# Kernel tuning notes

Hardware: AMD Instinct MI355X
Metric: run time of the kernel (lower is better)

## Reference

```python
import jax, jax.numpy as jnp
import numpy as np

K = 5  # kNN neighbors (includes self, as in PyG knn(x, x, k))


def _lin_bn(x, W, b, s, h):
    # Linear -> ReLU -> BatchNorm (inference, folded to scale s / shift h)
    return jax.nn.relu(x @ W + b) * s + h


def _knn_idx(x, k):
    # x: [B, N, F] -> idx: [B, N, k] indices of k nearest points (incl. self)
    x2 = jnp.sum(x * x, axis=-1)  # [B, N]
    d = x2[:, :, None] + x2[:, None, :] - 2.0 * jnp.einsum('bnf,bmf->bnm', x, x)
    return jax.lax.top_k(-d, k)[1]


def _edge_conv(x, k, edge_mlp):
    # DynamicEdgeConv: knn graph, message mlp([x_i, x_j - x_i]), max-aggregate
    idx = _knn_idx(x, k)                                   # [B, N, k]
    xj = jax.vmap(lambda xb, ib: xb[ib])(x, idx)           # [B, N, k, F]
    xi = jnp.broadcast_to(x[:, :, None, :], xj.shape)
    e = jnp.concatenate([xi, xj - xi], axis=-1)            # [B, N, k, 2F]
    return jnp.max(edge_mlp(e), axis=2)                    # [B, N, F_out]


def _forward(pos, w1a, b1a, s1a, h1a, w1b, b1b, s1b, h1b, w1c, b1c, s1c, h1c,
             w2, b2, s2, h2, wl, bl, sl, hl,
             wm1, bm1, sm1, hm1, wm2, bm2, sm2, hm2, wout, bout):
    mlp1 = lambda e: _lin_bn(_lin_bn(_lin_bn(e, w1a, b1a, s1a, h1a),
                                     w1b, b1b, s1b, h1b), w1c, b1c, s1c, h1c)
    mlp2 = lambda e: _lin_bn(e, w2, b2, s2, h2)
    x1 = _edge_conv(pos, K, mlp1)                          # [B, N, 64]
    x2 = _edge_conv(x1, K, mlp2)                           # [B, N, 128]
    out = _lin_bn(jnp.concatenate([x1, x2], axis=-1), wl, bl, sl, hl)  # [B,N,1024]
    out = jnp.max(out, axis=1)                             # global max pool -> [B,1024]
    out = _lin_bn(out, wm1, bm1, sm1, hm1)                 # Dropout = identity (eval)
    out = _lin_bn(out, wm2, bm2, sm2, hm2)
    return out @ wout + bout                               # [B, n_classes]


def setup_inputs() -> dict:
    key = jax.random.key(0)
    ks = jax.random.split(key, 32)
    B, N = 32, 2048
    rn = lambda k, sh: jax.random.normal(k, sh, dtype=jnp.float32)
    ru = lambda k, sh: jax.random.uniform(k, sh, dtype=jnp.float32)
    d = {'pos': rn(ks[0], (B, N, 3))}
    i = 1
    for nm, cin, cout in [('1a', 6, 64), ('1b', 64, 64), ('1c', 64, 64),
                          ('2', 128, 128), ('l', 192, 1024),
                          ('m1', 1024, 512), ('m2', 512, 256)]:
        d['w' + nm] = rn(ks[i], (cin, cout)) / np.sqrt(cin); i += 1
        d['b' + nm] = rn(ks[i], (cout,)) * 0.1; i += 1
        d['s' + nm] = ru(ks[i], (cout,)) + 0.5; i += 1
        d['h' + nm] = rn(ks[i], (cout,)) * 0.1; i += 1
    d['wout'] = rn(ks[i], (256, 2)) / np.sqrt(256.0); i += 1
    d['bout'] = rn(ks[i], (2,)) * 0.1
    return d


def reference(pos, w1a, b1a, s1a, h1a, w1b, b1b, s1b, h1b, w1c, b1c, s1c, h1c,
              w2, b2, s2, h2, wl, bl, sl, hl,
              wm1, bm1, sm1, hm1, wm2, bm2, sm2, hm2, wout, bout):
    return _forward(pos, w1a, b1a, s1a, h1a, w1b, b1b, s1b, h1b, w1c, b1c, s1c, h1c,
                    w2, b2, s2, h2, wl, bl, sl, hl,
                    wm1, bm1, sm1, hm1, wm2, bm2, sm2, hm2, wout, bout)
```

## Files before the change

### kernel.cpp

```cpp
#include <hip/hip_runtime.h>

#define DEV __device__ __forceinline__
DEV float relu_(float x) { return fmaxf(x, 0.0f); }

typedef __attribute__((ext_vector_type(4))) float f32x4;
typedef __attribute__((ext_vector_type(8))) __bf16 bf16x8;

DEV unsigned short bfbits(__bf16 b) { union { unsigned short s; __bf16 b; } x; x.b = b; return x.s; }
DEV __bf16 bffrom(unsigned short s) { union { unsigned short s; __bf16 b; } x; x.s = s; return x.b; }

DEV void knn_insert(float (&bd)[5], int (&bi)[5], float d, int j) {
  if (d >= bd[4]) return;
  bd[4] = d; bi[4] = j;
#pragma unroll
  for (int p = 4; p > 0; --p) {
    if (bd[p] < bd[p - 1]) {
      float td = bd[p]; bd[p] = bd[p - 1]; bd[p - 1] = td;
      int ti = bi[p]; bi[p] = bi[p - 1]; bi[p - 1] = ti;
    }
  }
}

DEV void knn_insert_bl(float (&bd)[5], int (&bi)[5], float d, int j) {
#pragma unroll
  for (int p = 0; p < 5; ++p) {
    bool lt = d < bd[p];
    float nd = lt ? d : bd[p];
    float cd = lt ? bd[p] : d;
    int ni = lt ? j : bi[p];
    int ci = lt ? bi[p] : j;
    bd[p] = nd; d = cd;
    bi[p] = ni; j = ci;
  }
}

DEV void ins5(float (&b)[5], float x) {
  b[4] = __builtin_amdgcn_fmed3f(b[3], b[4], x);
  b[3] = __builtin_amdgcn_fmed3f(b[2], b[3], x);
  b[2] = __builtin_amdgcn_fmed3f(b[1], b[2], x);
  b[1] = __builtin_amdgcn_fmed3f(b[0], b[1], x);
  b[0] = fminf(b[0], x);
}

__global__ __launch_bounds__(256) void k_front(
    const float* __restrict__ pos, const float* __restrict__ w1a,
    const float* __restrict__ b1a, const float* __restrict__ w1b,
    const float* __restrict__ w1c, const float* __restrict__ w2,
    const float* __restrict__ wl,
    int* __restrict__ idx1, float* __restrict__ uR, float* __restrict__ vR,
    __bf16* __restrict__ wfh, __bf16* __restrict__ wfl,
    __bf16* __restrict__ wph, __bf16* __restrict__ wpl,
    __bf16* __restrict__ wlb) {
  __shared__ __align__(16) float smem[9472];
  int tid = threadIdx.x;
  int blk = blockIdx.x;
  if (blk < 2048) {
    float* ps = smem;
    float* sqs = smem + 6144;
    float* md = smem + 8192;
    int* mi = (int*)(smem + 8832);
    int b = blk >> 6, qc = blk & 63;
    const float* src = pos + b * 6144;
    for (int u = tid; u < 6144; u += 256) ps[u] = src[u];
    __syncthreads();
    for (int u = tid; u < 2048; u += 256) {
      float x = ps[u * 3], y = ps[u * 3 + 1], z = ps[u * 3 + 2];
      sqs[u] = fmaf(z, z, fmaf(y, y, x * x));
    }
    __syncthreads();
    int q = tid & 31, sub = tid >> 5;
    int qi = qc * 32 + q;
    float qx = ps[qi * 3], qy = ps[qi * 3 + 1], qz = ps[qi * 3 + 2];
    float qsq = sqs[qi];
    float bp[5] = {1e30f, 1e30f, 1e30f, 1e30f, 1e30f};
    int j0 = sub * 256;
    for (int j = j0; j < j0 + 256; ++j) {
      float px = ps[j * 3], py = ps[j * 3 + 1], pz = ps[j * 3 + 2];
      float dot = fmaf(qz, pz, fmaf(qy, py, qx * px));
      float d = fmaxf((qsq + sqs[j]) - 2.0f * dot, 0.0f);
      unsigned u = (__float_as_uint(d) & 0xFFFFFF00u) | (unsigned)(j & 255);
      ins5(bp, __uint_as_float(u));
    }
    float bd[5]; int bi[5];
#pragma unroll
    for (int k = 0; k < 5; ++k) {
      unsigned u = __float_as_uint(bp[k]);
      bd[k] = __uint_as_float(u & 0xFFFFFF00u);
      bi[k] = j0 + (int)(u & 255u);
    }
    for (int half = 4; half >= 1; half >>= 1) {
      __syncthreads();
      if (sub >= half && sub < 2 * half) {
        int slot = (q * 4 + (sub - half)) * 5;
#pragma unroll
        for (int k = 0; k < 5; ++k) { md[slot + k] = bd[k]; mi[slot + k] = bi[k]; }
      }
      __syncthreads();
      if (sub < half) {
        int slot = (q * 4 + sub) * 5;
#pragma unroll
        for (int k = 0; k < 5; ++k) knn_insert_bl(bd, bi, md[slot + k], mi[slot + k]);
      }
    }
    if (sub == 0) {
      int* op = idx1 + (b * 2048 + qi) * 5;
#pragma unroll
      for (int k = 0; k < 5; ++k) op[k] = bi[k];
    }
  } else if (blk < 3072) {
    float* wAs = smem;
    float* bs = smem + 384;
    float* uS = smem + 448;
    float* vS = smem + 4800;
    for (int u = tid; u < 384; u += 256) wAs[u] = w1a[u];
    if (tid < 64) bs[tid] = b1a[tid];
    __syncthreads();
    int lane = tid & 63, fq = tid >> 6;
    int p0 = (blk - 2048) * 64;
    int p = p0 + lane;
    float x0 = pos[p * 3], x1 = pos[p * 3 + 1], x2 = pos[p * 3 + 2];
#pragma unroll
    for (int m = 0; m < 16; ++m) {
      int f = fq * 16 + m;
      float wt0 = wAs[f], wt1 = wAs[64 + f], wt2 = wAs[128 + f];
      float wb0 = wAs[192 + f], wb1 = wAs[256 + f], wb2 = wAs[320 + f];
      float uval = bs[f];
      uval = fmaf(x0, wt0 - wb0, uval);
      uval = fmaf(x1, wt1 - wb1, uval);
      uval = fmaf(x2, wt2 - wb2, uval);
      uS[lane * 68 + f] = uval;
      vS[lane * 68 + f] = fmaf(x2, wb2, fmaf(x1, wb1, x0 * wb0));
    }
    __syncthreads();
#pragma unroll
    for (int it = 0; it < 4; ++it) {
      int g = it * 1024 + tid * 4;
      int pl = g >> 6, f = g & 63;
      float4 uu = *(const float4*)(uS + pl * 68 + f);
      float4 vv = *(const float4*)(vS + pl * 68 + f);
      *(float4*)(uR + (size_t)p0 * 64 + g) = uu;
      *(float4*)(vR + (size_t)p0 * 64 + g) = vv;
    }
  } else {
    int pblk = blk - 3072;
    if (pblk < 4) {
      int t = pblk * 256 + tid;
      int m = t >> 9;
      int rem = t & 511;
      int nb = rem >> 7;
      int rem2 = rem & 127;
      int s = rem2 >> 6, lane = rem2 & 63;
      int k0 = s * 32 + (lane >> 4) * 8;
      int c = nb * 16 + (lane & 15);
      const float* W = m ? w1c : w1b;
      __bf16 oh[8], ol[8];
#pragma unroll
      for (int j = 0; j < 8; ++j) {
        float val = W[(k0 + j) * 64 + c];
        __bf16 h = (__bf16)val;
        oh[j] = h;
        ol[j] = (__bf16)(val - (float)h);
      }
      size_t off = (size_t)m * 4096 + ((size_t)((nb * 2 + s) * 64 + lane)) * 8;
      *(uint4*)(wfh + off) = *(const uint4*)oh;
      *(uint4*)(wfl + off) = *(const uint4*)ol;
    } else if (pblk < 12) {
      int t = (pblk - 4) * 256 + tid;
      int nb = t >> 7;
      int rem = t & 127;
      int ks = rem >> 6, lane = rem & 63;
      int k0 = ks * 32 + (lane >> 4) * 8;
      int col16 = lane & 15;
      __bf16 oh[8], ol[8];
#pragma unroll
      for (int j = 0; j < 8; ++j) {
        int k = k0 + j;
        float val;
        if (nb < 8) {
          int c = nb * 16 + col16;
          val = w2[k * 128 + c] - w2[(64 + k) * 128 + c];
        } else {
          int c = (nb - 8) * 16 + col16;
          val = w2[(64 + k) * 128 + c];
        }
        __bf16 h = (__bf16)val;
        oh[j] = h;
        ol[j] = (__bf16)(val - (float)h);
      }
      *(uint4*)(wph + (size_t)t * 8) = *(const uint4*)oh;
      *(uint4*)(wpl + (size_t)t * 8) = *(const uint4*)ol;
    } else {
      int t = (pblk - 12) * 256 + tid;
      int nt = t / 3072;
      int rem = t - nt * 3072;
      int ks = rem / 512;
      int rem2 = rem - ks * 512;
      int nb = rem2 >> 6, lane = rem2 & 63;
      int k0 = ks * 32 + (lane >> 4) * 8;
      int n = nt * 128 + nb * 16 + (lane & 15);
      __bf16 o[8];
#pragma unroll
      for (int j = 0; j < 8; ++j) o[j] = (__bf16)wl[(k0 + j) * 1024 + n];
      *(uint4*)(wlb + (size_t)t * 8) = *(const uint4*)o;
    }
  }
}

__global__ __launch_bounds__(256) void k_edge1(
    const int* __restrict__ idx1, const float* __restrict__ uR,
    const float* __restrict__ vR,
    const float* __restrict__ s1a, const float* __restrict__ h1a,
    const float* __restrict__ b1b, const float* __restrict__ s1b,
    const float* __restrict__ h1b,
    const float* __restrict__ b1c, const float* __restrict__ s1c,
    const float* __restrict__ h1c,
    const __bf16* __restrict__ wfh, const __bf16* __restrict__ wfl,
    __bf16* __restrict__ xh, __bf16* __restrict__ xl,
    float* __restrict__ sqo, __bf16* __restrict__ xb) {
  __shared__ __align__(16) __bf16 Wh[8192], Wl[8192];
  __shared__ __align__(16) unsigned h2b[4 * 1088];
  int tid = threadIdx.x;
  int w = tid >> 6, lane = tid & 63;
  int quad = lane >> 4, lm = lane & 15;
#pragma unroll
  for (int it = 0; it < 4; ++it) {
    int u4 = it * 256 + tid;
    *(uint4*)(Wh + (size_t)u4 * 8) = *(const uint4*)(wfh + (size_t)u4 * 8);
    *(uint4*)(Wl + (size_t)u4 * 8) = *(const uint4*)(wfl + (size_t)u4 * 8);
  }
  int p0 = blockIdx.x * 64;
  int b = p0 >> 11;
  size_t bb = (size_t)b * 2048;
  int edge = p0 + w * 16 + lm;
  float sA[2][8], hA[2][8];
#pragma unroll
  for (int s = 0; s < 2; ++s)
#pragma unroll
    for (int j = 0; j < 8; ++j) {
      int k = s * 32 + quad * 8 + j;
      sA[s][j] = s1a[k]; hA[s][j] = h1a[k];
    }
  float bB[4], sB[4], hB[4], bC[4], sC[4], hC[4];
#pragma unroll
  for (int nb = 0; nb < 4; ++nb) {
    int c = nb * 16 + lm;
    bB[nb] = b1b[c]; sB[nb] = s1b[c]; hB[nb] = h1b[c];
    bC[nb] = b1c[c]; sC[nb] = s1c[c]; hC[nb] = h1c[c];
  }
  unsigned* h2w = h2b + w * 1088;
  f32x4 mmax[4];
#pragma unroll
  for (int nb = 0; nb < 4; ++nb)
    mmax[nb] = (f32x4){-3.4e38f, -3.4e38f, -3.4e38f, -3.4e38f};
  __syncthreads();
  const float* urow = uR + (size_t)edge * 64;
  for (int kk = 0; kk < 5; ++kk) {
    int jn = idx1[edge * 5 + kk];
    const float* vrow = vR + (bb + jn) * 64;
    bf16x8 Ah[2], Al[2];
#pragma unroll
    for (int s = 0; s < 2; ++s) {
      int off = s * 32 + quad * 8;
      float4 u0 = *(const float4*)(urow + off);
      float4 u1 = *(const float4*)(urow + off + 4);
      float4 v0 = *(const float4*)(vrow + off);
      float4 v1 = *(const float4*)(vrow + off + 4);
      float uv[8] = {u0.x + v0.x, u0.y + v0.y, u0.z + v0.z, u0.w + v0.w,
                     u1.x + v1.x, u1.y + v1.y, u1.z + v1.z, u1.w + v1.w};
      __bf16 th[8], tl[8];
#pragma unroll
      for (int j = 0; j < 8; ++j) {
        float val = relu_(uv[j]) * sA[s][j] + hA[s][j];
        __bf16 hb = (__bf16)val;
        th[j] = hb;
        tl[j] = (__bf16)(val - (float)hb);
      }
      Ah[s] = *(const bf16x8*)th;
      Al[s] = *(const bf16x8*)tl;
    }
#pragma unroll
    for (int nb = 0; nb < 4; ++nb) {
      bf16x8 Bh0 = *(const bf16x8*)(Wh + ((size_t)((nb * 2 + 0) * 64 + lane)) * 8);
      bf16x8 Bh1 = *(const bf16x8*)(Wh + ((size_t)((nb * 2 + 1) * 64 + lane)) * 8);
      bf16x8 Bl0 = *(const bf16x8*)(Wl + ((size_t)((nb * 2 + 0) * 64 + lane)) * 8);
      bf16x8 Bl1 = *(const bf16x8*)(Wl + ((size_t)((nb * 2 + 1) * 64 + lane)) * 8);
      f32x4 a2 = {0.f, 0.f, 0.f, 0.f};
      a2 = __builtin_amdgcn_mfma_f32_16x16x32_bf16(Ah[0], Bh0, a2, 0, 0, 0);
      a2 = __builtin_amdgcn_mfma_f32_16x16x32_bf16(Ah[1], Bh1, a2, 0, 0, 0);
      a2 = __builtin_amdgcn_mfma_f32_16x16x32_bf16(Ah[0], Bl0, a2, 0, 0, 0);
      a2 = __builtin_amdgcn_mfma_f32_16x16x32_bf16(Ah[1], Bl1, a2, 0, 0, 0);
      a2 = __builtin_amdgcn_mfma_f32_16x16x32_bf16(Al[0], Bh0, a2, 0, 0, 0);
      a2 = __builtin_amdgcn_mfma_f32_16x16x32_bf16(Al[1], Bh1, a2, 0, 0, 0);
#pragma unroll
      for (int r = 0; r < 4; ++r) {
        float vv2 = relu_(a2[r] + bB[nb]) * sB[nb] + hB[nb];
        __bf16 hb = (__bf16)vv2;
        __bf16 lb = (__bf16)(vv2 - (float)hb);
        h2w[(quad * 4 + r) * 68 + nb * 16 + lm] =
            (unsigned)bfbits(hb) | ((unsigned)bfbits(lb) << 16);
      }
    }
    bf16x8 A3h[2], A3l[2];
#pragma unroll
    for (int s = 0; s < 2; ++s) {
      const unsigned* rp = h2w + lm * 68 + s * 32 + quad * 8;
      uint4 da = *(const uint4*)rp;
      uint4 db = *(const uint4*)(rp + 4);
      unsigned dw[8] = {da.x, da.y, da.z, da.w, db.x, db.y, db.z, db.w};
      __bf16 th[8], tl[8];
#pragma unroll
      for (int j = 0; j < 8; ++j) {
        th[j] = bffrom((unsigned short)(dw[j] & 0xFFFFu));
        tl[j] = bffrom((unsigned short)(dw[j] >> 16));
      }
      A3h[s] = *(const bf16x8*)th;
      A3l[s] = *(const bf16x8*)tl;
    }
#pragma unroll
    for (int nb = 0; nb < 4; ++nb) {
      bf16x8 Bh0 = *(const bf16x8*)(Wh + 4096 + ((size_t)((nb * 2 + 0) * 64 + lane)) * 8);
      bf16x8 Bh1 = *(const bf16x8*)(Wh + 4096 + ((size_t)((nb * 2 + 1) * 64 + lane)) * 8);
      bf16x8 Bl0 = *(const bf16x8*)(Wl + 4096 + ((size_t)((nb * 2 + 0) * 64 + lane)) * 8);
      bf16x8 Bl1 = *(const bf16x8*)(Wl + 4096 + ((size_t)((nb * 2 + 1) * 64 + lane)) * 8);
      f32x4 a3 = {0.f, 0.f, 0.f, 0.f};
      a3 = __builtin_amdgcn_mfma_f32_16x16x32_bf16(A3h[0], Bh0, a3, 0, 0, 0);
      a3 = __builtin_amdgcn_mfma_f32_16x16x32_bf16(A3h[1], Bh1, a3, 0, 0, 0);
      a3 = __builtin_amdgcn_mfma_f32_16x16x32_bf16(A3h[0], Bl0, a3, 0, 0, 0);
      a3 = __builtin_amdgcn_mfma_f32_16x16x32_bf16(A3h[1], Bl1, a3, 0, 0, 0);
      a3 = __builtin_amdgcn_mfma_f32_16x16x32_bf16(A3l[0], Bh0, a3, 0, 0, 0);
      a3 = __builtin_amdgcn_mfma_f32_16x16x32_bf16(A3l[1], Bh1, a3, 0, 0, 0);
#pragma unroll
      for (int r = 0; r < 4; ++r) mmax[nb][r] = fmaxf(mmax[nb][r], a3[r]);
    }
  }
  float sqp[4] = {0.f, 0.f, 0.f, 0.f};
#pragma unroll
  for (int nb = 0; nb < 4; ++nb) {
    int c = nb * 16 + lm;
#pragma unroll
    for (int r = 0; r < 4; ++r) {
      float vv3 = relu_(mmax[nb][r] + bC[nb]) * sC[nb] + hC[nb];
      sqp[r] = fmaf(vv3, vv3, sqp[r]);
      __bf16 hb = (__bf16)vv3;
      __bf16 lb = (__bf16)(vv3 - (float)hb);
      int n = p0 + w * 16 + quad * 4 + r;
      xh[(size_t)n * 64 + c] = hb;
      xl[(size_t)n * 64 + c] = lb;
      xb[(size_t)n * 192 + c] = hb;
    }
  }
#pragma unroll
  for (int r = 0; r < 4; ++r) {
    float s = sqp[r];
    s += __shfl_xor(s, 1);
    s += __shfl_xor(s, 2);
    s += __shfl_xor(s, 4);
    s += __shfl_xor(s, 8);
    if (lm == 0) sqo[p0 + w * 16 + quad * 4 + r] = s;
  }
}

__global__ __launch_bounds__(256) void k_mid(const __bf16* __restrict__ xh,
                                             const __bf16* __restrict__ xl,
                                             const float* __restrict__ sq,
                                             int* __restrict__ idx2,
                                             const __bf16* __restrict__ wph,
                                             const __bf16* __restrict__ wpl,
                                             __bf16* __restrict__ Pb,
                                             __bf16* __restrict__ Qb) {
  __shared__ __align__(16) float smem[6656];
  int tid = threadIdx.x;
  int w = tid >> 6, lane = tid & 63;
  int quad = lane >> 4, lm = lane & 15;
  if (blockIdx.x < 1024) {
    __bf16* Bh = (__bf16*)smem;
    __bf16* Bl = (__bf16*)(smem + 2304);
    float* sqs = smem + 4608;
    int b = blockIdx.x >> 5, qc = blockIdx.x & 31;
    int q0 = qc * 64;
    size_t bb = (size_t)b * 2048;
    for (int u = tid; u < 512; u += 256)
      *(float4*)(sqs + u * 4) = *(const float4*)(sq + bb + u * 4);
    const __bf16* qh = xh + (bb + q0 + w * 16 + lm) * 64 + quad * 8;
    const __bf16* ql = xl + (bb + q0 + w * 16 + lm) * 64 + quad * 8;
    bf16x8 Ah0 = *(const bf16x8*)(qh);
    bf16x8 Ah1 = *(const bf16x8*)(qh + 32);
    bf16x8 Al0 = *(const bf16x8*)(ql);
    bf16x8 Al1 = *(const bf16x8*)(ql + 32);
    __syncthreads();
    float qsq[4];
#pragma unroll
    for (int r = 0; r < 4; ++r) qsq[r] = sqs[q0 + w * 16 + quad * 4 + r];
    float bp[4][5];
#pragma unroll
    for (int r = 0; r < 4; ++r)
#pragma unroll
      for (int k = 0; k < 5; ++k) bp[r][k] = 1e30f;
    for (int ct = 0; ct < 32; ++ct) {
#pragma unroll
      for (int pass = 0; pass < 2; ++pass) {
        int unit = pass * 256 + tid;
        int n = unit >> 3, cc = unit & 7;
        const __bf16* gsrc = xh + (bb + ct * 64 + n) * 64 + cc * 8;
        const __bf16* gsrl = xl + (bb + ct * 64 + n) * 64 + cc * 8;
        *(uint4*)(Bh + n * 72 + cc * 8) = *(const uint4*)gsrc;
        *(uint4*)(Bl + n * 72 + cc * 8) = *(const uint4*)gsrl;
      }
      __syncthreads();
#pragma unroll
      for (int nt = 0; nt < 4; ++nt) {
        const __bf16* bph = Bh + (nt * 16 + lm) * 72 + quad * 8;
        const __bf16* bpl = Bl + (nt * 16 + lm) * 72 + quad * 8;
        bf16x8 Bh0 = *(const bf16x8*)(bph);
        bf16x8 Bh1 = *(const bf16x8*)(bph + 32);
        bf16x8 Bl0 = *(const bf16x8*)(bpl);
        bf16x8 Bl1 = *(const bf16x8*)(bpl + 32);
        f32x4 acc = {0.f, 0.f, 0.f, 0.f};
        acc = __builtin_amdgcn_mfma_f32_16x16x32_bf16(Ah0, Bh0, acc, 0, 0, 0);
        acc = __builtin_amdgcn_mfma_f32_16x16x32_bf16(Ah1, Bh1, acc, 0, 0, 0);
        acc = __builtin_amdgcn_mfma_f32_16x16x32_bf16(Ah0, Bl0, acc, 0, 0, 0);
        acc = __builtin_amdgcn_mfma_f32_16x16x32_bf16(Ah1, Bl1, acc, 0, 0, 0);
        acc = __builtin_amdgcn_mfma_f32_16x16x32_bf16(Al0, Bh0, acc, 0, 0, 0);
        acc = __builtin_amdgcn_mfma_f32_16x16x32_bf16(Al1, Bh1, acc, 0, 0, 0);
        int cid = ct * 64 + nt * 16 + lm;
        float csq = sqs[cid];
        unsigned key = (unsigned)(ct * 4 + nt);
#pragma unroll
        for (int r = 0; r < 4; ++r) {
          float d = fmaxf((qsq[r] + csq) - 2.0f * acc[r], 0.0f);
          unsigned u = (__float_as_uint(d) & 0xFFFFFF80u) | key;
          ins5(bp[r], __uint_as_float(u));
        }
      }
      __syncthreads();
    }
    float bd[4][5];
    int bi[4][5];
#pragma unroll
    for (int r = 0; r < 4; ++r)
#pragma unroll
      for (int k = 0; k < 5; ++k) {
        unsigned u = __float_as_uint(bp[r][k]);
        bd[r][k] = __uint_as_float(u & 0xFFFFFF80u);
        bi[r][k] = (int)((u & 0x7Fu) << 4) | lm;
      }
    for (int m = 1; m <= 8; m <<= 1) {
#pragma unroll
      for (int r = 0; r < 4; ++r) {
        float od[5]; int oi[5];
#pragma unroll
        for (int k = 0; k < 5; ++k) {
          od[k] = __shfl_xor(bd[r][k], m);
          oi[k] = __shfl_xor(bi[r][k], m);
        }
#pragma unroll
        for (int k = 0; k < 5; ++k) knn_insert(bd[r], bi[r], od[k], oi[k]);
      }
    }
    if (lm == 0) {
#pragma unroll
      for (int r = 0; r < 4; ++r) {
        int qi = q0 + w * 16 + quad * 4 + r;
        int* op = idx2 + (bb + qi) * 5;
#pragma unroll
        for (int k = 0; k < 5; ++k) op[k] = bi[r][k];
      }
    }
  } else {
    __bf16* Wh = (__bf16*)smem;
    __bf16* Wl = (__bf16*)(smem + 2048);
    int n0 = (blockIdx.x - 1024) * 64;
    const __bf16* ah = xh + (size_t)(n0 + w * 16 + lm) * 64 + quad * 8;
    const __bf16* al = xl + (size_t)(n0 + w * 16 + lm) * 64 + quad * 8;
    bf16x8 Ah0 = *(const bf16x8*)(ah);
    bf16x8 Ah1 = *(const bf16x8*)(ah + 32);
    bf16x8 Al0 = *(const bf16x8*)(al);
    bf16x8 Al1 = *(const bf16x8*)(al + 32);
    for (int chunk = 0; chunk < 4; ++chunk) {
      __syncthreads();
#pragma unroll
      for (int it = 0; it < 2; ++it) {
        int unit = it * 256 + tid;
        *(uint4*)(Wh + (size_t)unit * 8) =
            *(const uint4*)(wph + (size_t)chunk * 4096 + (size_t)unit * 8);
        *(uint4*)(Wl + (size_t)unit * 8) =
            *(const uint4*)(wpl + (size_t)chunk * 4096 + (size_t)unit * 8);
      }
      __syncthreads();
#pragma unroll
      for (int nb4 = 0; nb4 < 4; ++nb4) {
        int nb = chunk * 4 + nb4;
        bf16x8 Bh0 = *(const bf16x8*)(Wh + ((size_t)(nb4 * 2 + 0) * 64 + lane) * 8);
        bf16x8 Bh1 = *(const bf16x8*)(Wh + ((size_t)(nb4 * 2 + 1) * 64 + lane) * 8);
        bf16x8 Bl0 = *(const bf16x8*)(Wl + ((size_t)(nb4 * 2 + 0) * 64 + lane) * 8);
        bf16x8 Bl1 = *(const bf16x8*)(Wl + ((size_t)(nb4 * 2 + 1) * 64 + lane) * 8);
        f32x4 acc = {0.f, 0.f, 0.f, 0.f};
        acc = __builtin_amdgcn_mfma_f32_16x16x32_bf16(Ah0, Bh0, acc, 0, 0, 0);
        acc = __builtin_amdgcn_mfma_f32_16x16x32_bf16(Ah1, Bh1, acc, 0, 0, 0);
        acc = __builtin_amdgcn_mfma_f32_16x16x32_bf16(Ah0, Bl0, acc, 0, 0, 0);
        acc = __builtin_amdgcn_mfma_f32_16x16x32_bf16(Ah1, Bl1, acc, 0, 0, 0);
        acc = __builtin_amdgcn_mfma_f32_16x16x32_bf16(Al0, Bh0, acc, 0, 0, 0);
        acc = __builtin_amdgcn_mfma_f32_16x16x32_bf16(Al1, Bh1, acc, 0, 0, 0);
        bool isP = (nb < 8);
        __bf16* base = isP ? Pb : Qb;
        int col = (isP ? nb : nb - 8) * 16 + lm;
#pragma unroll
        for (int r = 0; r < 4; ++r) {
          int n = n0 + w * 16 + quad * 4 + r;
          base[(size_t)n * 128 + col] = (__bf16)acc[r];
        }
      }
    }
  }
}

__global__ __launch_bounds__(256) void k_gmax(const __bf16* __restrict__ Pb,
                                              const __bf16* __restrict__ Qb,
                                              const int* __restrict__ idx2,
                                              const float* __restrict__ b2,
                                              const float* __restrict__ s2,
                                              const float* __restrict__ h2v,
                                              __bf16* __restrict__ xb) {
  int tid = threadIdx.x;
  int c4 = tid & 31, p = tid >> 5;
  int n = blockIdx.x * 8 + p;
  int b = n >> 11;
  const int* ip = idx2 + n * 5;
  int c0 = c4 * 4;
  float m[4] = {-3.4e38f, -3.4e38f, -3.4e38f, -3.4e38f};
#pragma unroll
  for (int k = 0; k < 5; ++k) {
    int j = ip[k];
    uint2 q = *(const uint2*)(Qb + ((size_t)(b * 2048 + j)) * 128 + c0);
    m[0] = fmaxf(m[0], (float)bffrom((unsigned short)(q.x & 0xFFFFu)));
    m[1] = fmaxf(m[1], (float)bffrom((unsigned short)(q.x >> 16)));
    m[2] = fmaxf(m[2], (float)bffrom((unsigned short)(q.y & 0xFFFFu)));
    m[3] = fmaxf(m[3], (float)bffrom((unsigned short)(q.y >> 16)));
  }
  uint2 pv = *(const uint2*)(Pb + (size_t)n * 128 + c0);
  float pvf[4] = {(float)bffrom((unsigned short)(pv.x & 0xFFFFu)),
                  (float)bffrom((unsigned short)(pv.x >> 16)),
                  (float)bffrom((unsigned short)(pv.y & 0xFFFFu)),
                  (float)bffrom((unsigned short)(pv.y >> 16))};
  __bf16 o[4];
#pragma unroll
  for (int i = 0; i < 4; ++i) {
    float v = pvf[i] + m[i] + b2[c0 + i];
    o[i] = (__bf16)(relu_(v) * s2[c0 + i] + h2v[c0 + i]);
  }
  uint2 ov;
  ov.x = (unsigned)bfbits(o[0]) | ((unsigned)bfbits(o[1]) << 16);
  ov.y = (unsigned)bfbits(o[2]) | ((unsigned)bfbits(o[3]) << 16);
  *(uint2*)(xb + (size_t)n * 192 + 64 + c0) = ov;
}

__global__ __launch_bounds__(256) void k_linl_mfma(const __bf16* __restrict__ xb,
                                                   const __bf16* __restrict__ wlb,
                                                   float* __restrict__ pool_part) {
  __shared__ __align__(16) __bf16 Aall[12288];
  __shared__ __align__(16) __bf16 Bl[8192];
  int tid = threadIdx.x;
  int w = tid >> 6, lane = tid & 63;
  int mg = blockIdx.x;
  int n0 = mg << 6;
  int quad = lane >> 4, lm = lane & 15;
#pragma unroll
  for (int it = 0; it < 6; ++it) {
    int unit = it * 256 + tid;
    int mb = unit / 384;
    int rem = unit - mb * 384;
    int ks = rem >> 6, ln = rem & 63;
    int lmm = ln & 15, qd = ln >> 4;
    const uint4* ga = (const uint4*)(xb + (size_t)(n0 + mb * 16 + lmm) * 192 + ks * 32 + qd * 8);
    *(uint4*)(Aall + ((size_t)(mb * 6 + ks) * 64 + ln) * 8) = *ga;
  }
  for (int ng = 0; ng < 4; ++ng) {
    f32x4 acc[4][4];
#pragma unroll
    for (int i = 0; i < 4; ++i)
#pragma unroll
      for (int j = 0; j < 4; ++j) acc[i][j] = (f32x4){0.f, 0.f, 0.f, 0.f};
    for (int ks = 0; ks < 6; ++ks) {
      __syncthreads();
#pragma unroll
      for (int nt2 = 0; nt2 < 2; ++nt2) {
#pragma unroll
        for (int u = 0; u < 2; ++u) {
          int unit = u * 256 + tid;
          const uint4* gb = (const uint4*)(wlb + ((size_t)((ng * 2 + nt2) * 6 + ks)) * 4096 + (size_t)unit * 8);
          *(uint4*)(Bl + (size_t)nt2 * 4096 + (size_t)unit * 8) = *gb;
        }
      }
      __syncthreads();
      bf16x8 af[4], bfr[4];
#pragma unroll
      for (int i = 0; i < 4; ++i)
        af[i] = *(const bf16x8*)(Aall + ((size_t)(i * 6 + ks) * 64 + lane) * 8);
      int nt2 = w >> 1, nbb = (w & 1) * 4;
#pragma unroll
      for (int j = 0; j < 4; ++j)
        bfr[j] = *(const bf16x8*)(Bl + (size_t)nt2 * 4096 + ((size_t)((nbb + j) * 64 + lane)) * 8);
#pragma unroll
      for (int i = 0; i < 4; ++i)
#pragma unroll
        for (int j = 0; j < 4; ++j)
          acc[i][j] = __builtin_amdgcn_mfma_f32_16x16x32_bf16(af[i], bfr[j], acc[i][j], 0, 0, 0);
    }
#pragma unroll
    for (int j = 0; j < 4; ++j) {
      float m = -3.4e38f;
#pragma unroll
      for (int i = 0; i < 4; ++i)
#pragma unroll
        for (int r = 0; r < 4; ++r) m = fmaxf(m, acc[i][j][r]);
      m = fmaxf(m, __shfl_xor(m, 16));
      m = fmaxf(m, __shfl_xor(m, 32));
      if (quad == 0) {
        int ch = ng * 256 + (w >> 1) * 128 + (w & 1) * 64 + j * 16 + lm;
        pool_part[(size_t)mg * 1024 + ch] = m;
      }
    }
  }
}

__global__ __launch_bounds__(256) void k_pool(const float* __restrict__ pool_part,
                                              const float* __restrict__ bl,
                                              const float* __restrict__ sl,
                                              const float* __restrict__ hl,
                                              float* __restrict__ p,
                                              float* __restrict__ out) {
  int b = blockIdx.x >> 2, cb = blockIdx.x & 3;
  int c = cb * 256 + threadIdx.x;
  const float* src = pool_part + (size_t)(b * 32) * 1024 + c;
  float m0 = -3.4e38f, m1 = -3.4e38f, m2 = -3.4e38f, m3 = -3.4e38f;
#pragma unroll
  for (int t = 0; t < 32; t += 4) {
    m0 = fmaxf(m0, src[(size_t)t * 1024]);
    m1 = fmaxf(m1, src[(size_t)(t + 1) * 1024]);
    m2 = fmaxf(m2, src[(size_t)(t + 2) * 1024]);
    m3 = fmaxf(m3, src[(size_t)(t + 3) * 1024]);
  }
  float m = fmaxf(fmaxf(m0, m1), fmaxf(m2, m3));
  p[b * 1024 + c] = relu_(m + bl[c]) * sl[c] + hl[c];
  if (blockIdx.x == 0 && threadIdx.x < 64) out[threadIdx.x] = 0.0f;
}

__global__ __launch_bounds__(256) void k_m1(const float* __restrict__ p,
                                            const float* __restrict__ wm1,
                                            const float* __restrict__ bm1,
                                            const float* __restrict__ sm1,
                                            const float* __restrict__ hm1,
                                            float* __restrict__ h1) {
  __shared__ float p_s[1024];
  __shared__ float red[4][64];
  int b = blockIdx.x >> 3, cb = blockIdx.x & 7;
  int tid = threadIdx.x;
  for (int u = tid; u < 1024; u += 256) p_s[u] = p[b * 1024 + u];
  __syncthreads();
  int c64 = tid & 63, q = tid >> 6;
  int C = cb * 64 + c64;
  int f0 = q * 256;
  const float* W = wm1 + (size_t)f0 * 512 + C;
  float a[8] = {0.f, 0.f, 0.f, 0.f, 0.f, 0.f, 0.f, 0.f};
  for (int f = 0; f < 256; f += 8) {
#pragma unroll
    for (int u = 0; u < 8; ++u)
      a[u] = fmaf(p_s[f0 + f + u], W[(size_t)(f + u) * 512], a[u]);
  }
  red[q][c64] = ((a[0] + a[1]) + (a[2] + a[3])) + ((a[4] + a[5]) + (a[6] + a[7]));
  __syncthreads();
  if (tid < 64) {
    float t = (red[0][tid] + red[1][tid]) + (red[2][tid] + red[3][tid]);
    int C2 = cb * 64 + tid;
    h1[b * 512 + C2] = relu_(t + bm1[C2]) * sm1[C2] + hm1[C2];
  }
}

__global__ __launch_bounds__(256) void k_m2o(const float* __restrict__ h1,
                                             const float* __restrict__ wm2,
                                             const float* __restrict__ bm2,
                                             const float* __restrict__ sm2,
                                             const float* __restrict__ hm2,
                                             const float* __restrict__ wout,
                                             const float* __restrict__ bout,
                                             float* __restrict__ out) {
  __shared__ float h1_s[512];
  __shared__ float red[4][64];
  int b = blockIdx.x >> 2, cb = blockIdx.x & 3;
  int tid = threadIdx.x;
  for (int u = tid; u < 512; u += 256) h1_s[u] = h1[b * 512 + u];
  __syncthreads();
  int c64 = tid & 63, q = tid >> 6;
  int C = cb * 64 + c64;
  int f0 = q * 128;
  const float* W = wm2 + (size_t)f0 * 256 + C;
  float a[4] = {0.f, 0.f, 0.f, 0.f};
  for (int f = 0; f < 128; f += 4) {
#pragma unroll
    for (int u = 0; u < 4; ++u)
      a[u] = fmaf(h1_s[f0 + f + u], W[(size_t)(f + u) * 256], a[u]);
  }
  red[q][c64] = (a[0] + a[1]) + (a[2] + a[3]);
  __syncthreads();
  if (tid < 64) {
    float t = (red[0][tid] + red[1][tid]) + (red[2][tid] + red[3][tid]);
    int C2 = cb * 64 + tid;
    float h2v = relu_(t + bm2[C2]) * sm2[C2] + hm2[C2];
    float2 wv = *(const float2*)(wout + C2 * 2);
    float v0 = h2v * wv.x, v1 = h2v * wv.y;
#pragma unroll
    for (int m = 1; m < 64; m <<= 1) {
      v0 += __shfl_xor(v0, m);
      v1 += __shfl_xor(v1, m);
    }
    if (tid == 0) {
      if (cb == 0) { v0 += bout[0]; v1 += bout[1]; }
      atomicAdd(&out[b * 2], v0);
      atomicAdd(&out[b * 2 + 1], v1);
    }
  }
}

extern "C" void kernel_launch(void* const* d_in, const int* in_sizes, int n_in,
                              void* d_out, int out_size, void* d_ws, size_t ws_size,
                              hipStream_t stream) {
  const float* pos = (const float*)d_in[0];
  const float* w1a = (const float*)d_in[1];
  const float* b1a = (const float*)d_in[2];
  const float* s1a = (const float*)d_in[3];
  const float* h1a = (const float*)d_in[4];
  const float* w1b = (const float*)d_in[5];
  const float* b1b = (const float*)d_in[6];
  const float* s1b = (const float*)d_in[7];
  const float* h1b = (const float*)d_in[8];
  const float* w1c = (const float*)d_in[9];
  const float* b1c = (const float*)d_in[10];
  const float* s1c = (const float*)d_in[11];
  const float* h1c = (const float*)d_in[12];
  const float* w2 = (const float*)d_in[13];
  const float* b2 = (const float*)d_in[14];
  const float* s2 = (const float*)d_in[15];
  const float* h2 = (const float*)d_in[16];
  const float* wl = (const float*)d_in[17];
  const float* bl = (const float*)d_in[18];
  const float* sl = (const float*)d_in[19];
  const float* hl = (const float*)d_in[20];
  const float* wm1 = (const float*)d_in[21];
  const float* bm1 = (const float*)d_in[22];
  const float* sm1 = (const float*)d_in[23];
  const float* hm1 = (const float*)d_in[24];
  const float* wm2 = (const float*)d_in[25];
  const float* bm2 = (const float*)d_in[26];
  const float* sm2 = (const float*)d_in[27];
  const float* hm2 = (const float*)d_in[28];
  const float* wout = (const float*)d_in[29];
  const float* bout = (const float*)d_in[30];
  float* out = (float*)d_out;

  float* base = (float*)d_ws;
  __bf16* xh = (__bf16*)base;
  __bf16* xl = (__bf16*)(base + 2097152);
  float* PbF = base + 4194304;
  float* QbF = PbF + 4194304;
  float* xbF = QbF + 4194304;
  int* idx = (int*)(xbF + 6291456);
  float* sq = (float*)(idx + 327680);
  __bf16* wph = (__bf16*)(sq + 65536);
  __bf16* wpl = (__bf16*)(sq + 65536 + 8192);
  __bf16* wfh = (__bf16*)(sq + 65536 + 16384);
  __bf16* wfl = (__bf16*)(sq + 65536 + 20480);
  __bf16* wlb = (__bf16*)(sq + 65536 + 24576);
  __bf16* Pb = (__bf16*)PbF;
  __bf16* Qb = (__bf16*)QbF;
  __bf16* xb = (__bf16*)xbF;
  float* uR = PbF;
  float* vR = QbF;
  float* pool_part = base + 131072;
  float* p_pool = base + 1179648;
  float* h1g = base + 1212416;

  k_front<<<3180, 256, 0, stream>>>(pos, w1a, b1a, w1b, w1c, w2, wl, idx, uR, vR,
                                    wfh, wfl, wph, wpl, wlb);
  k_edge1<<<1024, 256, 0, stream>>>(idx, uR, vR, s1a, h1a, b1b, s1b, h1b, b1c,
                                    s1c, h1c, wfh, wfl, xh, xl, sq, xb);
  k_mid<<<2048, 256, 0, stream>>>(xh, xl, sq, idx, wph, wpl, Pb, Qb);
  k_gmax<<<8192, 256, 0, stream>>>(Pb, Qb, idx, b2, s2, h2, xb);
  k_linl_mfma<<<1024, 256, 0, stream>>>(xb, wlb, pool_part);
  k_pool<<<128, 256, 0, stream>>>(pool_part, bl, sl, hl, p_pool, out);
  k_m1<<<256, 256, 0, stream>>>(p_pool, wm1, bm1, sm1, hm1, h1g);
  k_m2o<<<128, 256, 0, stream>>>(h1g, wm2, bm2, sm2, hm2, wout, bout, out);
}
```

Measured before the change: 358.8 us.

## Split k_mid candidate scan across two thread groups with shared-memory top-k merge

k_mid now launches 512 threads per block. Two 256-thread groups each scan half of the candidate tiles (or half of the weight chunks in the projection branch) using their own shared-memory buffers. In the kNN branch, group 1 writes its per-row top-5 into shared memory and group 0 merges it before writing indices. This doubles per-block parallelism to shorten the serial candidate loop. In exchange it shrinks the key field in the packed distance to 6 bits, costs an extra merge and barrier, and raises shared-memory and register pressure per block.

```diff
diff --git a/kernel.cpp b/kernel.cpp
--- a/kernel.cpp
+++ b/kernel.cpp
@@ -360,7 +360,7 @@
   }
 }
 
-__global__ __launch_bounds__(256) void k_mid(const __bf16* __restrict__ xh,
+__global__ __launch_bounds__(512) void k_mid(const __bf16* __restrict__ xh,
                                              const __bf16* __restrict__ xl,
                                              const float* __restrict__ sq,
                                              int* __restrict__ idx2,
@@ -368,21 +368,23 @@
                                              const __bf16* __restrict__ wpl,
                                              __bf16* __restrict__ Pb,
                                              __bf16* __restrict__ Qb) {
-  __shared__ __align__(16) float smem[6656];
+  __shared__ __align__(16) float smem[11264];
   int tid = threadIdx.x;
-  int w = tid >> 6, lane = tid & 63;
+  int g = tid >> 8;
+  int t = tid & 255;
+  int ww = t >> 6;
+  int lane = tid & 63;
   int quad = lane >> 4, lm = lane & 15;
   if (blockIdx.x < 1024) {
-    __bf16* Bh = (__bf16*)smem;
-    __bf16* Bl = (__bf16*)(smem + 2304);
-    float* sqs = smem + 4608;
+    __bf16* Bh = (__bf16*)(smem + g * 4608);
+    __bf16* Bl = (__bf16*)(smem + g * 4608 + 2304);
+    float* sqs = smem + 9216;
     int b = blockIdx.x >> 5, qc = blockIdx.x & 31;
     int q0 = qc * 64;
     size_t bb = (size_t)b * 2048;
-    for (int u = tid; u < 512; u += 256)
-      *(float4*)(sqs + u * 4) = *(const float4*)(sq + bb + u * 4);
-    const __bf16* qh = xh + (bb + q0 + w * 16 + lm) * 64 + quad * 8;
-    const __bf16* ql = xl + (bb + q0 + w * 16 + lm) * 64 + quad * 8;
+    *(float4*)(sqs + tid * 4) = *(const float4*)(sq + bb + tid * 4);
+    const __bf16* qh = xh + (bb + q0 + ww * 16 + lm) * 64 + quad * 8;
+    const __bf16* ql = xl + (bb + q0 + ww * 16 + lm) * 64 + quad * 8;
     bf16x8 Ah0 = *(const bf16x8*)(qh);
     bf16x8 Ah1 = *(const bf16x8*)(qh + 32);
     bf16x8 Al0 = *(const bf16x8*)(ql);
@@ -390,16 +392,17 @@
     __syncthreads();
     float qsq[4];
 #pragma unroll
-    for (int r = 0; r < 4; ++r) qsq[r] = sqs[q0 + w * 16 + quad * 4 + r];
+    for (int r = 0; r < 4; ++r) qsq[r] = sqs[q0 + ww * 16 + quad * 4 + r];
     float bp[4][5];
 #pragma unroll
     for (int r = 0; r < 4; ++r)
 #pragma unroll
       for (int k = 0; k < 5; ++k) bp[r][k] = 1e30f;
-    for (int ct = 0; ct < 32; ++ct) {
+    for (int it = 0; it < 16; ++it) {
+      int ct = g * 16 + it;
 #pragma unroll
       for (int pass = 0; pass < 2; ++pass) {
-        int unit = pass * 256 + tid;
+        int unit = pass * 256 + t;
         int n = unit >> 3, cc = unit & 7;
         const __bf16* gsrc = xh + (bb + ct * 64 + n) * 64 + cc * 8;
         const __bf16* gsrl = xl + (bb + ct * 64 + n) * 64 + cc * 8;
@@ -422,13 +425,12 @@
         acc = __builtin_amdgcn_mfma_f32_16x16x32_bf16(Ah1, Bl1, acc, 0, 0, 0);
         acc = __builtin_amdgcn_mfma_f32_16x16x32_bf16(Al0, Bh0, acc, 0, 0, 0);
         acc = __builtin_amdgcn_mfma_f32_16x16x32_bf16(Al1, Bh1, acc, 0, 0, 0);
-        int cid = ct * 64 + nt * 16 + lm;
-        float csq = sqs[cid];
-        unsigned key = (unsigned)(ct * 4 + nt);
+        float csq = sqs[ct * 64 + nt * 16 + lm];
+        unsigned key = (unsigned)(it * 4 + nt);
 #pragma unroll
         for (int r = 0; r < 4; ++r) {
           float d = fmaxf((qsq[r] + csq) - 2.0f * acc[r], 0.0f);
-          unsigned u = (__float_as_uint(d) & 0xFFFFFF80u) | key;
+          unsigned u = (__float_as_uint(d) & 0xFFFFFFC0u) | key;
           ins5(bp[r], __uint_as_float(u));
         }
       }
@@ -441,8 +443,8 @@
 #pragma unroll
       for (int k = 0; k < 5; ++k) {
         unsigned u = __float_as_uint(bp[r][k]);
-        bd[r][k] = __uint_as_float(u & 0xFFFFFF80u);
-        bi[r][k] = (int)((u & 0x7Fu) << 4) | lm;
+        bd[r][k] = __uint_as_float(u & 0xFFFFFFC0u);
+        bi[r][k] = (((int)(u & 63u)) << 4) + lm + (g << 10);
       }
     for (int m = 1; m <= 8; m <<= 1) {
 #pragma unroll
@@ -457,30 +459,50 @@
         for (int k = 0; k < 5; ++k) knn_insert(bd[r], bi[r], od[k], oi[k]);
       }
     }
-    if (lm == 0) {
+    float* md = smem;
+    int* mi = (int*)(smem + 320);
+    if (g == 1 && lm == 0) {
 #pragma unroll
       for (int r = 0; r < 4; ++r) {
-        int qi = q0 + w * 16 + quad * 4 + r;
-        int* op = idx2 + (bb + qi) * 5;
-#pragma unroll
-        for (int k = 0; k < 5; ++k) op[k] = bi[r][k];
+        int row = ww * 16 + quad * 4 + r;
+#pragma unroll
+        for (int k = 0; k < 5; ++k) { md[row * 5 + k] = bd[r][k]; mi[row * 5 + k] = bi[r][k]; }
+      }
+    }
+    __syncthreads();
+    if (g == 0) {
+#pragma unroll
+      for (int r = 0; r < 4; ++r) {
+        int row = ww * 16 + quad * 4 + r;
+#pragma unroll
+        for (int k = 0; k < 5; ++k) knn_insert(bd[r], bi[r], md[row * 5 + k], mi[row * 5 + k]);
+      }
+      if (lm == 0) {
+#pragma unroll
+        for (int r = 0; r < 4; ++r) {
+          int qi = q0 + ww * 16 + quad * 4 + r;
+          int* op = idx2 + (bb + qi) * 5;
+#pragma unroll
+          for (int k = 0; k < 5; ++k) op[k] = bi[r][k];
+        }
       }
     }
   } else {
-    __bf16* Wh = (__bf16*)smem;
-    __bf16* Wl = (__bf16*)(smem + 2048);
+    __bf16* Wh = (__bf16*)(smem + g * 4096);
+    __bf16* Wl = (__bf16*)(smem + g * 4096 + 2048);
     int n0 = (blockIdx.x - 1024) * 64;
-    const __bf16* ah = xh + (size_t)(n0 + w * 16 + lm) * 64 + quad * 8;
-    const __bf16* al = xl + (size_t)(n0 + w * 16 + lm) * 64 + quad * 8;
+    const __bf16* ah = xh + (size_t)(n0 + ww * 16 + lm) * 64 + quad * 8;
+    const __bf16* al = xl + (size_t)(n0 + ww * 16 + lm) * 64 + quad * 8;
     bf16x8 Ah0 = *(const bf16x8*)(ah);
     bf16x8 Ah1 = *(const bf16x8*)(ah + 32);
     bf16x8 Al0 = *(const bf16x8*)(al);
     bf16x8 Al1 = *(const bf16x8*)(al + 32);
-    for (int chunk = 0; chunk < 4; ++chunk) {
+    for (int c2 = 0; c2 < 2; ++c2) {
+      int chunk = g * 2 + c2;
       __syncthreads();
 #pragma unroll
       for (int it = 0; it < 2; ++it) {
-        int unit = it * 256 + tid;
+        int unit = it * 256 + t;
         *(uint4*)(Wh + (size_t)unit * 8) =
             *(const uint4*)(wph + (size_t)chunk * 4096 + (size_t)unit * 8);
         *(uint4*)(Wl + (size_t)unit * 8) =
@@ -506,7 +528,7 @@
         int col = (isP ? nb : nb - 8) * 16 + lm;
 #pragma unroll
         for (int r = 0; r < 4; ++r) {
-          int n = n0 + w * 16 + quad * 4 + r;
+          int n = n0 + ww * 16 + quad * 4 + r;
           base[(size_t)n * 128 + col] = (__bf16)acc[r];
         }
       }
@@ -783,7 +805,7 @@
                                     wfh, wfl, wph, wpl, wlb);
   k_edge1<<<1024, 256, 0, stream>>>(idx, uR, vR, s1a, h1a, b1b, s1b, h1b, b1c,
                                     s1c, h1c, wfh, wfl, xh, xl, sq, xb);
-  k_mid<<<2048, 256, 0, stream>>>(xh, xl, sq, idx, wph, wpl, Pb, Qb);
+  k_mid<<<2048, 512, 0, stream>>>(xh, xl, sq, idx, wph, wpl, Pb, Qb);
   k_gmax<<<8192, 256, 0, stream>>>(Pb, Qb, idx, b2, s2, h2, xb);
   k_linl_mfma<<<1024, 256, 0, stream>>>(xb, wlb, pool_part);
   k_pool<<<128, 256, 0, stream>>>(pool_part, bl, sl, hl, p_pool, out);
```

Measured after the change: 375.0 us. 1.04x slower.

## Split second kNN candidate range across two blocks and merge partial top-5

Applied to the files above, without the earlier changes.

The second-layer kNN search now divides each query tile's 2048 candidates into two halves handled by separate blocks, which doubles the kNN grid from 1024 to 2048 blocks. Each block writes its partial top-5 distances and indices into an unused region of the xb buffer, and a new small kernel merges the two lists into the final indices. The aim is more parallelism and shorter per-block serial loops for better GPU occupancy. The cost is an extra kernel launch, scratch traffic, and one fewer key bit in the packed distance (mask 0xFFFFFFC0), which slightly coarsens distance precision.

```diff
diff --git a/kernel.cpp b/kernel.cpp
--- a/kernel.cpp
+++ b/kernel.cpp
@@ -363,7 +363,7 @@
 __global__ __launch_bounds__(256) void k_mid(const __bf16* __restrict__ xh,
                                              const __bf16* __restrict__ xl,
                                              const float* __restrict__ sq,
-                                             int* __restrict__ idx2,
+                                             __bf16* __restrict__ scratch,
                                              const __bf16* __restrict__ wph,
                                              const __bf16* __restrict__ wpl,
                                              __bf16* __restrict__ Pb,
@@ -372,11 +372,14 @@
   int tid = threadIdx.x;
   int w = tid >> 6, lane = tid & 63;
   int quad = lane >> 4, lm = lane & 15;
-  if (blockIdx.x < 1024) {
+  if (blockIdx.x < 2048) {
     __bf16* Bh = (__bf16*)smem;
     __bf16* Bl = (__bf16*)(smem + 2304);
     float* sqs = smem + 4608;
-    int b = blockIdx.x >> 5, qc = blockIdx.x & 31;
+    int blk = blockIdx.x;
+    int b = blk >> 6;
+    int w6 = blk & 63;
+    int qc = w6 >> 1, g = w6 & 1;
     int q0 = qc * 64;
     size_t bb = (size_t)b * 2048;
     for (int u = tid; u < 512; u += 256)
@@ -396,7 +399,8 @@
     for (int r = 0; r < 4; ++r)
 #pragma unroll
       for (int k = 0; k < 5; ++k) bp[r][k] = 1e30f;
-    for (int ct = 0; ct < 32; ++ct) {
+    for (int it = 0; it < 16; ++it) {
+      int ct = g * 16 + it;
 #pragma unroll
       for (int pass = 0; pass < 2; ++pass) {
         int unit = pass * 256 + tid;
@@ -422,13 +426,12 @@
         acc = __builtin_amdgcn_mfma_f32_16x16x32_bf16(Ah1, Bl1, acc, 0, 0, 0);
         acc = __builtin_amdgcn_mfma_f32_16x16x32_bf16(Al0, Bh0, acc, 0, 0, 0);
         acc = __builtin_amdgcn_mfma_f32_16x16x32_bf16(Al1, Bh1, acc, 0, 0, 0);
-        int cid = ct * 64 + nt * 16 + lm;
-        float csq = sqs[cid];
-        unsigned key = (unsigned)(ct * 4 + nt);
+        float csq = sqs[ct * 64 + nt * 16 + lm];
+        unsigned key = (unsigned)(it * 4 + nt);
 #pragma unroll
         for (int r = 0; r < 4; ++r) {
           float d = fmaxf((qsq[r] + csq) - 2.0f * acc[r], 0.0f);
-          unsigned u = (__float_as_uint(d) & 0xFFFFFF80u) | key;
+          unsigned u = (__float_as_uint(d) & 0xFFFFFFC0u) | key;
           ins5(bp[r], __uint_as_float(u));
         }
       }
@@ -441,8 +444,8 @@
 #pragma unroll
       for (int k = 0; k < 5; ++k) {
         unsigned u = __float_as_uint(bp[r][k]);
-        bd[r][k] = __uint_as_float(u & 0xFFFFFF80u);
-        bi[r][k] = (int)((u & 0x7Fu) << 4) | lm;
+        bd[r][k] = __uint_as_float(u & 0xFFFFFFC0u);
+        bi[r][k] = (g << 10) + (((int)(u & 63u)) << 4) + lm;
       }
     for (int m = 1; m <= 8; m <<= 1) {
 #pragma unroll
@@ -461,15 +464,20 @@
 #pragma unroll
       for (int r = 0; r < 4; ++r) {
         int qi = q0 + w * 16 + quad * 4 + r;
-        int* op = idx2 + (bb + qi) * 5;
-#pragma unroll
-        for (int k = 0; k < 5; ++k) op[k] = bi[r][k];
+        uint2* sp = (uint2*)((char*)scratch + (size_t)(bb + qi) * 384 + 128 + g * 40);
+#pragma unroll
+        for (int k = 0; k < 5; ++k) {
+          uint2 v;
+          v.x = __float_as_uint(bd[r][k]);
+          v.y = (unsigned)bi[r][k];
+          sp[k] = v;
+        }
       }
     }
   } else {
     __bf16* Wh = (__bf16*)smem;
     __bf16* Wl = (__bf16*)(smem + 2048);
-    int n0 = (blockIdx.x - 1024) * 64;
+    int n0 = (blockIdx.x - 2048) * 64;
     const __bf16* ah = xh + (size_t)(n0 + w * 16 + lm) * 64 + quad * 8;
     const __bf16* al = xl + (size_t)(n0 + w * 16 + lm) * 64 + quad * 8;
     bf16x8 Ah0 = *(const bf16x8*)(ah);
@@ -512,6 +520,27 @@
       }
     }
   }
+}
+
+__global__ __launch_bounds__(256) void k_kmerge(const __bf16* __restrict__ scratch,
+                                                int* __restrict__ idx2) {
+  int n = blockIdx.x * 256 + threadIdx.x;
+  const uint2* sp = (const uint2*)((const char*)scratch + (size_t)n * 384 + 128);
+  float bd[5]; int bi[5];
+#pragma unroll
+  for (int k = 0; k < 5; ++k) {
+    uint2 v = sp[k];
+    bd[k] = __uint_as_float(v.x);
+    bi[k] = (int)v.y;
+  }
+#pragma unroll
+  for (int k = 0; k < 5; ++k) {
+    uint2 v = sp[5 + k];
+    knn_insert(bd, bi, __uint_as_float(v.x), (int)v.y);
+  }
+  int* op = idx2 + (size_t)n * 5;
+#pragma unroll
+  for (int k = 0; k < 5; ++k) op[k] = bi[k];
 }
 
 __global__ __launch_bounds__(256) void k_gmax(const __bf16* __restrict__ Pb,
@@ -783,7 +812,8 @@
                                     wfh, wfl, wph, wpl, wlb);
   k_edge1<<<1024, 256, 0, stream>>>(idx, uR, vR, s1a, h1a, b1b, s1b, h1b, b1c,
                                     s1c, h1c, wfh, wfl, xh, xl, sq, xb);
-  k_mid<<<2048, 256, 0, stream>>>(xh, xl, sq, idx, wph, wpl, Pb, Qb);
+  k_mid<<<3072, 256, 0, stream>>>(xh, xl, sq, xb, wph, wpl, Pb, Qb);
+  k_kmerge<<<256, 256, 0, stream>>>(xb, idx);
   k_gmax<<<8192, 256, 0, stream>>>(Pb, Qb, idx, b2, s2, h2, xb);
   k_linl_mfma<<<1024, 256, 0, stream>>>(xb, wlb, pool_part);
   k_pool<<<128, 256, 0, stream>>>(pool_part, bl, sl, hl, p_pool, out);
```

After: 363.2 us. No clear change (+1.2%).
